# Optimization experiments

Hardware: AMD Instinct MI355X
Metric: run time of the kernel (lower is better)

## Reference

```python
import jax, jax.numpy as jnp
import numpy as np

N_NODES = 50000
N_EDGES = 800000
IN_CH = 64
HID = 128
LAST_HID = 256


def setup_inputs() -> dict:
    key = jax.random.key(0)
    ks = jax.random.split(key, 12)
    x = jax.random.normal(ks[0], (N_NODES, IN_CH), dtype=jnp.float32)
    edge_index = jax.random.randint(ks[1], (2, N_EDGES), 0, N_NODES, dtype=jnp.int64)
    s = lambda fan_in: 1.0 / np.sqrt(fan_in)
    return {
        "x": x,
        "edge_index": edge_index,
        # SAGEConv1: lin_l (aggregated neighbors, with bias), lin_r (root, no bias)
        "W1l": jax.random.normal(ks[2], (HID, IN_CH), dtype=jnp.float32) * s(IN_CH),
        "b1l": jnp.zeros((HID,), dtype=jnp.float32),
        "W1r": jax.random.normal(ks[3], (HID, IN_CH), dtype=jnp.float32) * s(IN_CH),
        # SAGEConv2 -> 1 channel
        "W2l": jax.random.normal(ks[4], (1, HID), dtype=jnp.float32) * s(HID),
        "b2l": jnp.zeros((1,), dtype=jnp.float32),
        "W2r": jax.random.normal(ks[5], (1, HID), dtype=jnp.float32) * s(HID),
        # fc1 (LazyLinear bound to N_NODES input features) and fc2
        "fc1_W": jax.random.normal(ks[6], (LAST_HID, N_NODES), dtype=jnp.float32) * s(N_NODES),
        "fc1_b": jnp.zeros((LAST_HID,), dtype=jnp.float32),
        "fc2_W": jax.random.normal(ks[7], (1, LAST_HID), dtype=jnp.float32) * s(LAST_HID),
        "fc2_b": jnp.zeros((1,), dtype=jnp.float32),
    }


def _sage_conv(h, src, dst, Wl, bl, Wr, n_nodes):
    # PyG SAGEConv (mean aggr): out = lin_l(mean_{j in N(i)} x_j) + lin_r(x_i)
    msgs = h[src]  # [E, F] gather of source node features
    summed = jax.ops.segment_sum(msgs, dst, num_segments=n_nodes)  # [N, F]
    deg = jax.ops.segment_sum(jnp.ones((src.shape[0],), h.dtype), dst, num_segments=n_nodes)
    agg = summed / jnp.maximum(deg, 1.0)[:, None]
    return agg @ Wl.T + bl + h @ Wr.T


def reference(x, edge_index, W1l, b1l, W1r, W2l, b2l, W2r, fc1_W, fc1_b, fc2_W, fc2_b):
    n = x.shape[0]
    src, dst = edge_index[0], edge_index[1]
    h = jax.nn.relu(_sage_conv(x, src, dst, W1l, b1l, W1r, n))   # [N, HID]
    h = jax.nn.relu(_sage_conv(h, src, dst, W2l, b2l, W2r, n))   # [N, 1]
    v = h[:, 0]                                                   # [N]
    z = fc1_W @ v + fc1_b                                         # [LAST_HID]
    pred = fc2_W @ z + fc2_b                                      # [1]
    return pred[0]  # scalar (torch.squeeze)
```

## Files before the change

### kernel.cpp

```cpp
#include <hip/hip_runtime.h>

#define N_NODESC 50000
#define N_EDGESC 800000
#define MAXDEG 64

__global__ void k0_init(int* __restrict__ deg, float* __restrict__ z) {
    int i = blockIdx.x * 256 + threadIdx.x;
    if (i < N_NODESC) deg[i] = 0;
    if (i < 256) z[i] = 0.0f;
}

__global__ void k1_bucket(const int* __restrict__ ei, int* __restrict__ deg,
                          int* __restrict__ bucket) {
    int e = blockIdx.x * 256 + threadIdx.x;
    int src = ei[e];
    int dst = ei[N_EDGESC + e];
    int slot = atomicAdd(&deg[dst], 1);
    if (slot < MAXDEG) bucket[dst * MAXDEG + slot] = src;
}

__global__ void k2_agg(const float* __restrict__ x, const int* __restrict__ deg,
                       const int* __restrict__ bucket, float* __restrict__ agg) {
    int lane = threadIdx.x & 63;
    int node = blockIdx.x * 4 + (threadIdx.x >> 6);
    int g  = lane >> 4;
    int c4 = lane & 15;
    int d = deg[node];
    int c = min(d, MAXDEG);
    const int* brow = bucket + node * MAXDEG;
    float4 acc = make_float4(0.f, 0.f, 0.f, 0.f);
    int k = 0;
    for (; k + 8 <= c; k += 8) {
        int b0 = brow[k + g];
        int b1 = brow[k + 4 + g];
        float4 v0 = ((const float4*)(x + b0 * 64))[c4];
        float4 v1 = ((const float4*)(x + b1 * 64))[c4];
        acc.x += v0.x + v1.x; acc.y += v0.y + v1.y;
        acc.z += v0.z + v1.z; acc.w += v0.w + v1.w;
    }
    for (; k < c; k += 4) {
        if (k + g < c) {
            float4 v = ((const float4*)(x + brow[k + g] * 64))[c4];
            acc.x += v.x; acc.y += v.y; acc.z += v.z; acc.w += v.w;
        }
    }
    #pragma unroll
    for (int m = 16; m <= 32; m <<= 1) {
        acc.x += __shfl_xor(acc.x, m);
        acc.y += __shfl_xor(acc.y, m);
        acc.z += __shfl_xor(acc.z, m);
        acc.w += __shfl_xor(acc.w, m);
    }
    if (g == 0) {
        float inv = 1.0f / (float)max(d, 1);
        float4 r = make_float4(acc.x * inv, acc.y * inv, acc.z * inv, acc.w * inv);
        ((float4*)(agg + node * 64))[c4] = r;
    }
}

#define WS 68

__launch_bounds__(256, 3)
__global__ void k3_mm_fused(const float* __restrict__ x, const float* __restrict__ agg,
                            const float* __restrict__ W1l, const float* __restrict__ b1l,
                            const float* __restrict__ W1r,
                            const float* __restrict__ W2l, const float* __restrict__ W2r,
                            float* __restrict__ s_out, float* __restrict__ t_out) {
    __shared__ __align__(16) float sW[128 * WS];
    __shared__ __align__(16) float sXA[64 * WS];

    int tid = threadIdx.x;
    int tx = tid & 15;
    int ty = tid >> 4;
    int node0 = blockIdx.x * 64;

    float bR[8], lR[8], rR[8];
    #pragma unroll
    for (int oj = 0; oj < 8; oj++) {
        int o = tx + 16 * oj;
        bR[oj] = b1l[o]; lR[oj] = W2l[o]; rR[oj] = W2r[o];
    }

    float acc[4][8];
    #pragma unroll
    for (int i = 0; i < 4; i++)
        #pragma unroll
        for (int j = 0; j < 8; j++) acc[i][j] = 0.f;

    for (int ph = 0; ph < 2; ph++) {
        const float* Wsrc = (ph == 0) ? W1r : W1l;
        const float* Asrc = (ph == 0) ? x : agg;
        __syncthreads();
        for (int i = tid * 4; i < 128 * 64; i += 1024) {
            float4 w = *(const float4*)(Wsrc + i);
            int o = i >> 6, k = i & 63;
            *(float4*)&sW[o * WS + k] = w;
        }
        for (int i = tid * 4; i < 64 * 64; i += 1024) {
            int n = i >> 6, k = i & 63;
            int node = node0 + n;
            float4 a = make_float4(0.f, 0.f, 0.f, 0.f);
            if (node < N_NODESC) a = *(const float4*)(Asrc + node * 64 + k);
            *(float4*)&sXA[n * WS + k] = a;
        }
        __syncthreads();
        #pragma unroll 4
        for (int k = 0; k < 64; k += 4) {
            float4 a4[4], w4[8];
            #pragma unroll
            for (int ni = 0; ni < 4; ni++)
                a4[ni] = *(const float4*)&sXA[(ty + 16 * ni) * WS + k];
            #pragma unroll
            for (int oj = 0; oj < 8; oj++)
                w4[oj] = *(const float4*)&sW[(tx + 16 * oj) * WS + k];
            #pragma unroll
            for (int ni = 0; ni < 4; ni++)
                #pragma unroll
                for (int oj = 0; oj < 8; oj++)
                    acc[ni][oj] += a4[ni].x * w4[oj].x + a4[ni].y * w4[oj].y
                                 + a4[ni].z * w4[oj].z + a4[ni].w * w4[oj].w;
        }
    }

    #pragma unroll
    for (int ni = 0; ni < 4; ni++) {
        float sp = 0.f, tp = 0.f;
        #pragma unroll
        for (int oj = 0; oj < 8; oj++) {
            float h = fmaxf(acc[ni][oj] + bR[oj], 0.f);
            sp += h * lR[oj];
            tp += h * rR[oj];
        }
        #pragma unroll
        for (int m = 1; m <= 8; m <<= 1) {
            sp += __shfl_xor(sp, m);
            tp += __shfl_xor(tp, m);
        }
        if (tx == 0) {
            int node = node0 + ty + 16 * ni;
            if (node < N_NODESC) { s_out[node] = sp; t_out[node] = tp; }
        }
    }
}

__global__ void k4_layer2(const float* __restrict__ s, const float* __restrict__ t,
                          const int* __restrict__ deg, const int* __restrict__ bucket,
                          const float* __restrict__ b2l, float* __restrict__ v) {
    int tid = threadIdx.x;
    int lane = tid & 15;
    int node = blockIdx.x * 16 + (tid >> 4);
    int d = deg[node];
    int c = min(d, MAXDEG);
    float sum = 0.f;
    for (int k = lane; k < c; k += 16) sum += s[bucket[node * MAXDEG + k]];
    sum += __shfl_xor(sum, 1);
    sum += __shfl_xor(sum, 2);
    sum += __shfl_xor(sum, 4);
    sum += __shfl_xor(sum, 8);
    if (lane == 0) {
        float h = sum / (float)max(d, 1) + b2l[0] + t[node];
        v[node] = fmaxf(h, 0.f);
    }
}

__global__ void k5_fc1(const float* __restrict__ fc1W, const float* __restrict__ v,
                       float* __restrict__ z) {
    int row = blockIdx.x >> 2;
    int part = blockIdx.x & 3;
    const float4* W4 = (const float4*)(fc1W + row * 50000 + part * 12500);
    const float4* v4 = (const float4*)(v + part * 12500);
    float sum = 0.f;
    for (int i = threadIdx.x; i < 3125; i += 256) {
        float4 w = W4[i], a = v4[i];
        sum += w.x * a.x + w.y * a.y + w.z * a.z + w.w * a.w;
    }
    #pragma unroll
    for (int m = 1; m < 64; m <<= 1) sum += __shfl_xor(sum, m);
    __shared__ float red[4];
    if ((threadIdx.x & 63) == 0) red[threadIdx.x >> 6] = sum;
    __syncthreads();
    if (threadIdx.x == 0) atomicAdd(&z[row], red[0] + red[1] + red[2] + red[3]);
}

__global__ void k6_head(const float* __restrict__ z, const float* __restrict__ fc1b,
                        const float* __restrict__ fc2W, const float* __restrict__ fc2b,
                        float* __restrict__ out) {
    int t = threadIdx.x;
    float val = (z[t] + fc1b[t]) * fc2W[t];
    #pragma unroll
    for (int m = 1; m < 64; m <<= 1) val += __shfl_xor(val, m);
    __shared__ float red[4];
    if ((t & 63) == 0) red[t >> 6] = val;
    __syncthreads();
    if (t == 0) out[0] = red[0] + red[1] + red[2] + red[3] + fc2b[0];
}

extern "C" void kernel_launch(void* const* d_in, const int* in_sizes, int n_in,
                              void* d_out, int out_size, void* d_ws, size_t ws_size,
                              hipStream_t stream) {
    const float* x    = (const float*)d_in[0];
    const int*   ei   = (const int*)d_in[1];
    const float* W1l  = (const float*)d_in[2];
    const float* b1l  = (const float*)d_in[3];
    const float* W1r  = (const float*)d_in[4];
    const float* W2l  = (const float*)d_in[5];
    const float* b2l  = (const float*)d_in[6];
    const float* W2r  = (const float*)d_in[7];
    const float* fc1W = (const float*)d_in[8];
    const float* fc1b = (const float*)d_in[9];
    const float* fc2W = (const float*)d_in[10];
    const float* fc2b = (const float*)d_in[11];
    float* out = (float*)d_out;

    char* ws = (char*)d_ws;
    int*   deg    = (int*)  (ws + 0);
    float* z      = (float*)(ws + 200192);
    int*   bucket = (int*)  (ws + 201216);
    float* agg    = (float*)(ws + 13001216);
    float* s      = (float*)(ws + 25801216);
    float* t      = (float*)(ws + 26001216);
    float* v      = (float*)(ws + 26201216);

    k0_init   <<<196,   256, 0, stream>>>(deg, z);
    k1_bucket <<<3125,  256, 0, stream>>>(ei, deg, bucket);
    k2_agg    <<<12500, 256, 0, stream>>>(x, deg, bucket, agg);
    k3_mm_fused<<<782,  256, 0, stream>>>(x, agg, W1l, b1l, W1r, W2l, W2r, s, t);
    k4_layer2 <<<3125,  256, 0, stream>>>(s, t, deg, bucket, b2l, v);
    k5_fc1    <<<1024,  256, 0, stream>>>(fc1W, v, z);
    k6_head   <<<1,     256, 0, stream>>>(z, fc1b, fc2W, fc2b, out);
}
```

Measured before the change: 240.0 us.

## Partition edge bucketing by dst range, shuffle-broadcast neighbor ids, enlarge GEMM tile

The bucketing kernel now has each group of blocks scan a slice of edges and keep only edges whose destination falls in one of eight node ranges. This keeps the atomics and bucket writes for a group local to a smaller region, but every edge is read eight times. The aggregation kernel loads a node's 64 bucket entries once per wavefront and broadcasts neighbor indices with shuffles instead of reloading them. The fused layer-1 GEMM doubles its node tile to 128 per block, raising reuse of the weights held in shared memory. In exchange, register pressure rises and occupancy is capped at 2 blocks.

```diff
diff --git a/kernel.cpp b/kernel.cpp
--- a/kernel.cpp
+++ b/kernel.cpp
@@ -10,13 +10,23 @@
     if (i < 256) z[i] = 0.0f;
 }
 
+#define K1_BLOCKS 2048
+#define K1_EPB (N_EDGESC / (K1_BLOCKS / 8))
 __global__ void k1_bucket(const int* __restrict__ ei, int* __restrict__ deg,
                           int* __restrict__ bucket) {
-    int e = blockIdx.x * 256 + threadIdx.x;
-    int src = ei[e];
-    int dst = ei[N_EDGESC + e];
-    int slot = atomicAdd(&deg[dst], 1);
-    if (slot < MAXDEG) bucket[dst * MAXDEG + slot] = src;
+    int g   = blockIdx.x & 7;
+    int idx = blockIdx.x >> 3;
+    int lo = g * (N_NODESC / 8), hi = lo + (N_NODESC / 8);
+    int e0 = idx * K1_EPB;
+    for (int i = threadIdx.x; i < K1_EPB; i += 256) {
+        int e = e0 + i;
+        int dst = ei[N_EDGESC + e];
+        int src = ei[e];
+        if (dst >= lo && dst < hi) {
+            int slot = atomicAdd(&deg[dst], 1);
+            if (slot < MAXDEG) bucket[dst * MAXDEG + slot] = src;
+        }
+    }
 }
 
 __global__ void k2_agg(const float* __restrict__ x, const int* __restrict__ deg,
@@ -27,20 +37,18 @@
     int c4 = lane & 15;
     int d = deg[node];
     int c = min(d, MAXDEG);
-    const int* brow = bucket + node * MAXDEG;
+    int bidx = bucket[node * MAXDEG + lane];
     float4 acc = make_float4(0.f, 0.f, 0.f, 0.f);
-    int k = 0;
-    for (; k + 8 <= c; k += 8) {
-        int b0 = brow[k + g];
-        int b1 = brow[k + 4 + g];
-        float4 v0 = ((const float4*)(x + b0 * 64))[c4];
-        float4 v1 = ((const float4*)(x + b1 * 64))[c4];
-        acc.x += v0.x + v1.x; acc.y += v0.y + v1.y;
-        acc.z += v0.z + v1.z; acc.w += v0.w + v1.w;
-    }
-    for (; k < c; k += 4) {
-        if (k + g < c) {
-            float4 v = ((const float4*)(x + brow[k + g] * 64))[c4];
+    for (int k = 0; k < c; k += 8) {
+        int i0 = k + g, i1 = k + 4 + g;
+        int b0 = __shfl(bidx, i0);
+        int b1 = __shfl(bidx, i1);
+        if (i0 < c) {
+            float4 v = ((const float4*)(x + b0 * 64))[c4];
+            acc.x += v.x; acc.y += v.y; acc.z += v.z; acc.w += v.w;
+        }
+        if (i1 < c) {
+            float4 v = ((const float4*)(x + b1 * 64))[c4];
             acc.x += v.x; acc.y += v.y; acc.z += v.z; acc.w += v.w;
         }
     }
@@ -53,37 +61,33 @@
     }
     if (g == 0) {
         float inv = 1.0f / (float)max(d, 1);
-        float4 r = make_float4(acc.x * inv, acc.y * inv, acc.z * inv, acc.w * inv);
-        ((float4*)(agg + node * 64))[c4] = r;
+        ((float4*)(agg + node * 64))[c4] =
+            make_float4(acc.x * inv, acc.y * inv, acc.z * inv, acc.w * inv);
     }
 }
 
 #define WS 68
 
-__launch_bounds__(256, 3)
+__launch_bounds__(256, 2)
 __global__ void k3_mm_fused(const float* __restrict__ x, const float* __restrict__ agg,
                             const float* __restrict__ W1l, const float* __restrict__ b1l,
                             const float* __restrict__ W1r,
                             const float* __restrict__ W2l, const float* __restrict__ W2r,
                             float* __restrict__ s_out, float* __restrict__ t_out) {
     __shared__ __align__(16) float sW[128 * WS];
-    __shared__ __align__(16) float sXA[64 * WS];
+    __shared__ __align__(16) float sXA[128 * WS];
+    __shared__ float sB[128], sL[128], sR[128];
 
     int tid = threadIdx.x;
     int tx = tid & 15;
     int ty = tid >> 4;
-    int node0 = blockIdx.x * 64;
-
-    float bR[8], lR[8], rR[8];
-    #pragma unroll
-    for (int oj = 0; oj < 8; oj++) {
-        int o = tx + 16 * oj;
-        bR[oj] = b1l[o]; lR[oj] = W2l[o]; rR[oj] = W2r[o];
-    }
-
-    float acc[4][8];
-    #pragma unroll
-    for (int i = 0; i < 4; i++)
+    int node0 = blockIdx.x * 128;
+
+    if (tid < 128) { sB[tid] = b1l[tid]; sL[tid] = W2l[tid]; sR[tid] = W2r[tid]; }
+
+    float acc[8][8];
+    #pragma unroll
+    for (int i = 0; i < 8; i++)
         #pragma unroll
         for (int j = 0; j < 8; j++) acc[i][j] = 0.f;
 
@@ -91,12 +95,14 @@
         const float* Wsrc = (ph == 0) ? W1r : W1l;
         const float* Asrc = (ph == 0) ? x : agg;
         __syncthreads();
+        #pragma unroll
         for (int i = tid * 4; i < 128 * 64; i += 1024) {
             float4 w = *(const float4*)(Wsrc + i);
             int o = i >> 6, k = i & 63;
             *(float4*)&sW[o * WS + k] = w;
         }
-        for (int i = tid * 4; i < 64 * 64; i += 1024) {
+        #pragma unroll
+        for (int i = tid * 4; i < 128 * 64; i += 1024) {
             int n = i >> 6, k = i & 63;
             int node = node0 + n;
             float4 a = make_float4(0.f, 0.f, 0.f, 0.f);
@@ -104,17 +110,16 @@
             *(float4*)&sXA[n * WS + k] = a;
         }
         __syncthreads();
-        #pragma unroll 4
         for (int k = 0; k < 64; k += 4) {
-            float4 a4[4], w4[8];
+            float4 a4[8], w4[8];
             #pragma unroll
-            for (int ni = 0; ni < 4; ni++)
+            for (int ni = 0; ni < 8; ni++)
                 a4[ni] = *(const float4*)&sXA[(ty + 16 * ni) * WS + k];
             #pragma unroll
             for (int oj = 0; oj < 8; oj++)
                 w4[oj] = *(const float4*)&sW[(tx + 16 * oj) * WS + k];
             #pragma unroll
-            for (int ni = 0; ni < 4; ni++)
+            for (int ni = 0; ni < 8; ni++)
                 #pragma unroll
                 for (int oj = 0; oj < 8; oj++)
                     acc[ni][oj] += a4[ni].x * w4[oj].x + a4[ni].y * w4[oj].y
@@ -123,13 +128,14 @@
     }
 
     #pragma unroll
-    for (int ni = 0; ni < 4; ni++) {
+    for (int ni = 0; ni < 8; ni++) {
         float sp = 0.f, tp = 0.f;
         #pragma unroll
         for (int oj = 0; oj < 8; oj++) {
-            float h = fmaxf(acc[ni][oj] + bR[oj], 0.f);
-            sp += h * lR[oj];
-            tp += h * rR[oj];
+            int o = tx + 16 * oj;
+            float h = fmaxf(acc[ni][oj] + sB[o], 0.f);
+            sp += h * sL[o];
+            tp += h * sR[o];
         }
         #pragma unroll
         for (int m = 1; m <= 8; m <<= 1) {
@@ -222,9 +228,9 @@
     float* v      = (float*)(ws + 26201216);
 
     k0_init   <<<196,   256, 0, stream>>>(deg, z);
-    k1_bucket <<<3125,  256, 0, stream>>>(ei, deg, bucket);
+    k1_bucket <<<K1_BLOCKS, 256, 0, stream>>>(ei, deg, bucket);
     k2_agg    <<<12500, 256, 0, stream>>>(x, deg, bucket, agg);
-    k3_mm_fused<<<782,  256, 0, stream>>>(x, agg, W1l, b1l, W1r, W2l, W2r, s, t);
+    k3_mm_fused<<<391,  256, 0, stream>>>(x, agg, W1l, b1l, W1r, W2l, W2r, s, t);
     k4_layer2 <<<3125,  256, 0, stream>>>(s, t, deg, bucket, b2l, v);
     k5_fc1    <<<1024,  256, 0, stream>>>(fc1W, v, z);
     k6_head   <<<1,     256, 0, stream>>>(z, fc1b, fc2W, fc2b, out);
```

New measurement: 230.3 us. 1.04x faster.
